# Kernel optimization log

Hardware: AMD Instinct MI355X
Metric: run time of the kernel (lower is better)

The kernel has to match this reference:

```python
import jax, jax.numpy as jnp
import numpy as np


def setup_inputs() -> dict:
    key = jax.random.key(0)
    k1, k2 = jax.random.split(key)
    B, IN, OUT = 4096, 4096, 4096
    x = jax.random.normal(k1, (B, IN), dtype=jnp.float32)
    W = jax.random.normal(k2, (OUT, IN), dtype=jnp.float32) * (1.0 / np.sqrt(IN))
    return {"x": x, "W": W, "k": 128}


def reference(x, W, k):
    # temp = (x[:, None, :] * W).sum(axis=1)  ==  x * W.sum(axis=0)  -> [B, in]
    # (the original materializes the O(B*out*in) intermediate; math is identical)
    temp = jax.lax.stop_gradient(x) * jnp.sum(W, axis=0)  # x_vals is detached in torch
    _, idx_top = jax.lax.top_k(jnp.abs(temp), k)          # [B, k] indices into `in` dim
    B = x.shape[0]
    z = jnp.ones_like(x).at[jnp.arange(B)[:, None], idx_top].set(0.0)
    out = jnp.matmul(x * z, W.T)                          # [B, out]
    return out
```

## Files before the change

### kernel.cpp

```cpp
#include <hip/hip_runtime.h>
#include <hip/hip_bf16.h>
#include <stdint.h>

#define B_DIM   4096
#define IN_DIM  4096
#define OUT_DIM 4096
#define K_SEL   128

typedef unsigned short u16;
typedef __bf16 bf16x8 __attribute__((ext_vector_type(8)));
typedef float  f32x4  __attribute__((ext_vector_type(4)));

static __device__ __forceinline__ u16 f2bf(float f) {
    uint32_t u = __builtin_bit_cast(uint32_t, f);
    uint32_t r = (u + 0x7fffu + ((u >> 16) & 1u)) >> 16;
    return (u16)r;
}

__global__ __launch_bounds__(256) void colsum_conv(const float* __restrict__ W,
                                                   double* __restrict__ part,
                                                   u16* __restrict__ Wb) {
    int cb = blockIdx.x & 15;
    int rb = blockIdx.x >> 4;
    int col = cb * 256 + threadIdx.x;
    int row0 = rb * 32;
    double s = 0.0;
    for (int r = 0; r < 32; ++r) {
        size_t idx = (size_t)(row0 + r) * IN_DIM + col;
        float v = W[idx];
        s += (double)v;
        Wb[idx] = f2bf(v);
    }
    part[(size_t)rb * IN_DIM + col] = s;
}

__global__ __launch_bounds__(256) void colsum_final(const double* __restrict__ part,
                                                    float* __restrict__ cs) {
    int col = blockIdx.x * 256 + threadIdx.x;
    double s = 0.0;
    for (int r = 0; r < 128; ++r) s += part[(size_t)r * IN_DIM + col];
    cs[col] = (float)s;
}

__global__ __launch_bounds__(256) void topk_mask(const float* __restrict__ x,
                                                 const float* __restrict__ cs,
                                                 u16* __restrict__ xz) {
    __shared__ uint32_t hist[256];
    __shared__ uint32_t suf[256];
    __shared__ uint32_t s_scan[256];
    __shared__ uint32_t s_prefix, s_krem;

    const int b = blockIdx.x, t = threadIdx.x;
    const float4* xrow = (const float4*)(x + (size_t)b * IN_DIM);
    const float4* csv  = (const float4*)cs;

    float    xr[16];
    uint32_t ul[16];
#pragma unroll
    for (int q = 0; q < 4; ++q) {
        float4 xv = xrow[t * 4 + q];
        float4 cv = csv[t * 4 + q];
        xr[q*4+0] = xv.x; xr[q*4+1] = xv.y; xr[q*4+2] = xv.z; xr[q*4+3] = xv.w;
        ul[q*4+0] = __builtin_bit_cast(uint32_t, xv.x * cv.x) & 0x7fffffffu;
        ul[q*4+1] = __builtin_bit_cast(uint32_t, xv.y * cv.y) & 0x7fffffffu;
        ul[q*4+2] = __builtin_bit_cast(uint32_t, xv.z * cv.z) & 0x7fffffffu;
        ul[q*4+3] = __builtin_bit_cast(uint32_t, xv.w * cv.w) & 0x7fffffffu;
    }
    if (t == 0) { s_prefix = 0u; s_krem = K_SEL; }
    __syncthreads();

#pragma unroll
    for (int p = 3; p >= 0; --p) {
        const int sh = p * 8;
        const uint32_t hi_mask = (p == 3) ? 0u : (0xFFFFFFFFu << (sh + 8));
        const uint32_t prefix = s_prefix;
        const uint32_t krem   = s_krem;
        hist[t] = 0u;
        __syncthreads();
#pragma unroll
        for (int j = 0; j < 16; ++j) {
            uint32_t u = ul[j];
            if ((u & hi_mask) == (prefix & hi_mask))
                atomicAdd(&hist[(u >> sh) & 255u], 1u);
        }
        __syncthreads();
        uint32_t mine = hist[t];
        suf[t] = mine;
        __syncthreads();
#pragma unroll
        for (int off = 1; off < 256; off <<= 1) {
            uint32_t other = (t + off < 256) ? suf[t + off] : 0u;
            __syncthreads();
            mine += other;
            suf[t] = mine;
            __syncthreads();
        }
        uint32_t mysuf   = suf[t];
        uint32_t nextsuf = (t < 255) ? suf[t + 1] : 0u;
        if (mysuf >= krem && (t == 255 || nextsuf < krem)) {
            s_prefix = prefix | ((uint32_t)t << sh);
            s_krem   = krem - nextsuf;
        }
        __syncthreads();
    }
    const uint32_t T       = s_prefix;
    const uint32_t need_eq = s_krem;

    int cnt = 0;
#pragma unroll
    for (int j = 0; j < 16; ++j) cnt += (ul[j] == T) ? 1 : 0;
    s_scan[t] = (uint32_t)cnt;
    __syncthreads();
    uint32_t inc = (uint32_t)cnt;
#pragma unroll
    for (int off = 1; off < 256; off <<= 1) {
        uint32_t other = (t >= off) ? s_scan[t - off] : 0u;
        __syncthreads();
        inc += other;
        s_scan[t] = inc;
        __syncthreads();
    }
    const int base = (int)(inc - (uint32_t)cnt);

    union { u16 us[16]; uint4 v[2]; } ob;
    int eqseen = 0;
#pragma unroll
    for (int j = 0; j < 16; ++j) {
        uint32_t u = ul[j];
        bool drop = (u > T);
        if (u == T) {
            if (base + eqseen < (int)need_eq) drop = true;
            ++eqseen;
        }
        ob.us[j] = drop ? (u16)0 : f2bf(xr[j]);
    }
    uint4* dst = (uint4*)(xz + (size_t)b * IN_DIM + t * 16);
    dst[0] = ob.v[0];
    dst[1] = ob.v[1];
}

#define NT 64

__global__ __launch_bounds__(512, 2) void gemm_8ph(const u16* __restrict__ A,
                                                   const u16* __restrict__ Bm,
                                                   float* __restrict__ C) {
    __shared__ u16 lds_[65536];

    const int bid = blockIdx.x;
    const int swz = (bid & 7) * 32 + (bid >> 3);
    const int m0 = (swz >> 4) * 256, n0 = (swz & 15) * 256;

    const int t = threadIdx.x;
    const int w = t >> 6, l = t & 63;
    const int lr = l & 15, lk = l >> 4;
    const int wm = w >> 2, wn = w & 3;

    const int cswz = ((t & 7) ^ ((t >> 3) & 7)) * 8;
    const int colA = (lk * 8) ^ ((lr & 7) * 8);

    f32x4 acc[8][4];
#pragma unroll
    for (int i = 0; i < 8; ++i)
#pragma unroll
        for (int j = 0; j < 4; ++j) acc[i][j] = f32x4{0.f, 0.f, 0.f, 0.f};

#define GLOAD(g, off_bytes)                                                     \
    __builtin_amdgcn_global_load_lds(                                           \
        (const __attribute__((address_space(1))) void*)(g),                     \
        (__attribute__((address_space(3))) void*)(((char*)lds_) + (off_bytes)), \
        16, 0, 0)

    auto stA = [&](int kb, int s, int kt) {
        GLOAD(A + (size_t)(m0 + s * 64 + (t >> 3)) * IN_DIM + kt + cswz,
              kb * 65536 + s * 8192 + t * 16);
    };
    auto stB = [&](int kb, int s, int kt) {
        GLOAD(Bm + (size_t)(n0 + s * 64 + (t >> 3)) * IN_DIM + kt + cswz,
              kb * 65536 + 32768 + s * 8192 + t * 16);
    };

    stA(0, 0, 0); stA(0, 1, 0); stA(0, 2, 0); stA(0, 3, 0);
    stB(0, 0, 0); stB(0, 1, 0); stB(0, 2, 0); stB(0, 3, 0);
    stA(1, 0, 64); stA(1, 2, 64);
    asm volatile("s_waitcnt vmcnt(2)" ::: "memory");
    __builtin_amdgcn_s_barrier();
    asm volatile("" ::: "memory");

    for (int k = 0; k < NT; ++k) {
        const int buf = k & 1, bufn = buf ^ 1;
        const int kt1 = (k + 1) * 64;
        const int ktc = (k + 2 < NT ? k + 2 : NT - 1) * 64;
        const int Ab = buf * 32768 + (wm * 2) * 4096;
        const int Bb = buf * 32768 + 16384 + wn * 4096;
#pragma unroll
        for (int p = 0; p < 4; ++p) {
            const int q = p >> 1, ks = p & 1;
            const int col = colA ^ (ks * 32);
            bf16x8 a[4], b[4];
            const int ra = Ab + q * 4096 + lr * 64 + col;
#pragma unroll
            for (int mi = 0; mi < 4; ++mi)
                a[mi] = *(const bf16x8*)&lds_[ra + mi * 1024];
            const int rb = Bb + lr * 64 + col;
#pragma unroll
            for (int ni = 0; ni < 4; ++ni)
                b[ni] = *(const bf16x8*)&lds_[rb + ni * 1024];

            if (p == 0) {
                if (k < NT - 1) { stB(bufn, 0, kt1); stB(bufn, 1, kt1);
                                  stA(bufn, 1, kt1); stA(bufn, 3, kt1); }
            } else if (p == 1) {
                if (k < NT - 1) { stB(bufn, 2, kt1); stB(bufn, 3, kt1); }
            } else if (p == 2) {
                stA(buf, 0, ktc); stA(buf, 2, ktc);
            }
            asm volatile("" ::: "memory");
            __builtin_amdgcn_s_barrier();
            asm volatile("s_waitcnt lgkmcnt(0)" ::: "memory");
            __builtin_amdgcn_sched_barrier(0);
            __builtin_amdgcn_s_setprio(1);
#pragma unroll
            for (int mi = 0; mi < 4; ++mi)
#pragma unroll
                for (int ni = 0; ni < 4; ++ni)
                    acc[q * 4 + mi][ni] = __builtin_amdgcn_mfma_f32_16x16x32_bf16(
                        a[mi], b[ni], acc[q * 4 + mi][ni], 0, 0, 0);
            __builtin_amdgcn_s_setprio(0);
            __builtin_amdgcn_sched_barrier(0);
            if (p == 3) asm volatile("s_waitcnt vmcnt(2)" ::: "memory");
            asm volatile("" ::: "memory");
            __builtin_amdgcn_s_barrier();
            asm volatile("" ::: "memory");
        }
    }
#undef GLOAD

#pragma unroll
    for (int gmi = 0; gmi < 8; ++gmi)
#pragma unroll
        for (int ni = 0; ni < 4; ++ni)
#pragma unroll
            for (int r = 0; r < 4; ++r) {
                int row = m0 + wm * 128 + (gmi >> 2) * 64 + (gmi & 3) * 16 + lk * 4 + r;
                int col = n0 + wn * 64 + ni * 16 + lr;
                C[(size_t)row * OUT_DIM + col] = acc[gmi][ni][r];
            }
}

extern "C" void kernel_launch(void* const* d_in, const int* in_sizes, int n_in,
                              void* d_out, int out_size, void* d_ws, size_t ws_size,
                              hipStream_t stream) {
    const float* x = (const float*)d_in[0];
    const float* W = (const float*)d_in[1];
    float* out = (float*)d_out;

    char* ws = (char*)d_ws;
    u16*    Wb   = (u16*)ws;
    u16*    xz   = (u16*)(ws + (size_t)32 * 1024 * 1024);
    float*  cs   = (float*)(ws + (size_t)64 * 1024 * 1024);
    double* part = (double*)d_out;

    colsum_conv<<<2048, 256, 0, stream>>>(W, part, Wb);
    colsum_final<<<16, 256, 0, stream>>>(part, cs);
    topk_mask<<<4096, 256, 0, stream>>>(x, cs, xz);
    gemm_8ph<<<256, 512, 0, stream>>>(xz, Wb, out);
}
```

Before: 195.2 us.

## Restructure GEMM main loop into quadrant phases with register reuse of A/B fragments

Rewrites the bf16 GEMM inner loop so each K-tile runs four quadrant phases (A-top×B-left, A-top×B-right, A-bottom×B-left, A-bottom×B-right). Loaded A and B fragments are reused across phases, which cuts LDS reads per tile. The LDS layout and global-to-LDS load order change so the next tiles are prefetched per quadrant, interleaved with the MFMA blocks and tracked by new vmcnt/lgkmcnt waits. The aim is fewer LDS reads and better overlap of loads with MFMAs. The cost is more fragile synchronisation and higher register pressure from holding A and both B halves at once.

After: 189.3 us. -3.0%, faster.

```diff
diff --git a/kernel.cpp b/kernel.cpp
--- a/kernel.cpp
+++ b/kernel.cpp
@@ -156,7 +156,7 @@
     const int wm = w >> 2, wn = w & 3;
 
     const int cswz = ((t & 7) ^ ((t >> 3) & 7)) * 8;
-    const int colA = (lk * 8) ^ ((lr & 7) * 8);
+    const int c0   = (lk ^ (lr & 7)) * 8;
 
     f32x4 acc[8][4];
 #pragma unroll
@@ -169,71 +169,131 @@
         (const __attribute__((address_space(1))) void*)(g),                     \
         (__attribute__((address_space(3))) void*)(((char*)lds_) + (off_bytes)), \
         16, 0, 0)
-
-    auto stA = [&](int kb, int s, int kt) {
-        GLOAD(A + (size_t)(m0 + s * 64 + (t >> 3)) * IN_DIM + kt + cswz,
-              kb * 65536 + s * 8192 + t * 16);
+#define MFMA_(d, va, vb) d = __builtin_amdgcn_mfma_f32_16x16x32_bf16(va, vb, d, 0, 0, 0)
+
+    auto stA = [&](int b, int qm, int kt) {
+#pragma unroll
+        for (int g = 0; g < 2; ++g)
+            GLOAD(A + (size_t)(m0 + g * 128 + qm * 64 + (t >> 3)) * IN_DIM + kt + cswz,
+                  b * 65536 + qm * 16384 + g * 8192 + t * 16);
     };
-    auto stB = [&](int kb, int s, int kt) {
-        GLOAD(Bm + (size_t)(n0 + s * 64 + (t >> 3)) * IN_DIM + kt + cswz,
-              kb * 65536 + 32768 + s * 8192 + t * 16);
+    auto stB = [&](int b, int qn, int kt) {
+#pragma unroll
+        for (int g = 0; g < 2; ++g)
+            GLOAD(Bm + (size_t)(n0 + (g * 2 + (t >> 8)) * 64 + qn * 32 + ((t >> 3) & 31)) * IN_DIM + kt + cswz,
+                  b * 65536 + 32768 + qn * 16384 + g * 8192 + t * 16);
     };
 
-    stA(0, 0, 0); stA(0, 1, 0); stA(0, 2, 0); stA(0, 3, 0);
-    stB(0, 0, 0); stB(0, 1, 0); stB(0, 2, 0); stB(0, 3, 0);
-    stA(1, 0, 64); stA(1, 2, 64);
-    asm volatile("s_waitcnt vmcnt(2)" ::: "memory");
+    stA(0, 0, 0); stB(0, 0, 0); stA(0, 1, 0); stB(0, 1, 0);
+    stA(1, 0, 64); stB(1, 0, 64); stA(1, 1, 64);
+    asm volatile("s_waitcnt vmcnt(6)" ::: "memory");
     __builtin_amdgcn_s_barrier();
     asm volatile("" ::: "memory");
 
     for (int k = 0; k < NT; ++k) {
         const int buf = k & 1, bufn = buf ^ 1;
-        const int kt1 = (k + 1) * 64;
-        const int ktc = (k + 2 < NT ? k + 2 : NT - 1) * 64;
-        const int Ab = buf * 32768 + (wm * 2) * 4096;
-        const int Bb = buf * 32768 + 16384 + wn * 4096;
-#pragma unroll
-        for (int p = 0; p < 4; ++p) {
-            const int q = p >> 1, ks = p & 1;
-            const int col = colA ^ (ks * 32);
-            bf16x8 a[4], b[4];
-            const int ra = Ab + q * 4096 + lr * 64 + col;
-#pragma unroll
-            for (int mi = 0; mi < 4; ++mi)
-                a[mi] = *(const bf16x8*)&lds_[ra + mi * 1024];
-            const int rb = Bb + lr * 64 + col;
-#pragma unroll
-            for (int ni = 0; ni < 4; ++ni)
-                b[ni] = *(const bf16x8*)&lds_[rb + ni * 1024];
-
-            if (p == 0) {
-                if (k < NT - 1) { stB(bufn, 0, kt1); stB(bufn, 1, kt1);
-                                  stA(bufn, 1, kt1); stA(bufn, 3, kt1); }
-            } else if (p == 1) {
-                if (k < NT - 1) { stB(bufn, 2, kt1); stB(bufn, 3, kt1); }
-            } else if (p == 2) {
-                stA(buf, 0, ktc); stA(buf, 2, ktc);
-            }
-            asm volatile("" ::: "memory");
-            __builtin_amdgcn_s_barrier();
-            asm volatile("s_waitcnt lgkmcnt(0)" ::: "memory");
-            __builtin_amdgcn_sched_barrier(0);
-            __builtin_amdgcn_s_setprio(1);
-#pragma unroll
-            for (int mi = 0; mi < 4; ++mi)
-#pragma unroll
-                for (int ni = 0; ni < 4; ++ni)
-                    acc[q * 4 + mi][ni] = __builtin_amdgcn_mfma_f32_16x16x32_bf16(
-                        a[mi], b[ni], acc[q * 4 + mi][ni], 0, 0, 0);
-            __builtin_amdgcn_s_setprio(0);
-            __builtin_amdgcn_sched_barrier(0);
-            if (p == 3) asm volatile("s_waitcnt vmcnt(2)" ::: "memory");
-            asm volatile("" ::: "memory");
-            __builtin_amdgcn_s_barrier();
-            asm volatile("" ::: "memory");
-        }
+        const int kt1 = (k + 1 < NT ? k + 1 : NT - 1) * 64;
+        const int kt2 = (k + 2 < NT ? k + 2 : NT - 1) * 64;
+        const int aB = buf * 32768 + (wm * 64 + lr) * 64;
+        const int bB = buf * 32768 + 16384 + (wn * 32 + lr) * 64;
+
+        bf16x8 a[4][2], b0[2][2], b1[2][2];
+
+#pragma unroll
+        for (int mi = 0; mi < 4; ++mi) {
+            a[mi][0] = *(const bf16x8*)&lds_[aB + mi * 1024 + c0];
+            a[mi][1] = *(const bf16x8*)&lds_[aB + mi * 1024 + (c0 ^ 32)];
+        }
+#pragma unroll
+        for (int ni = 0; ni < 2; ++ni) {
+            b0[ni][0] = *(const bf16x8*)&lds_[bB + ni * 1024 + c0];
+            b0[ni][1] = *(const bf16x8*)&lds_[bB + ni * 1024 + (c0 ^ 32)];
+        }
+        stB(bufn, 1, kt1);
+        asm volatile("s_waitcnt lgkmcnt(8)" ::: "memory");
+        __builtin_amdgcn_s_barrier();
+        asm volatile("s_waitcnt lgkmcnt(0)" ::: "memory");
+        __builtin_amdgcn_sched_barrier(0);
+        __builtin_amdgcn_s_setprio(1);
+#pragma unroll
+        for (int mi = 0; mi < 4; ++mi)
+#pragma unroll
+            for (int ni = 0; ni < 2; ++ni) {
+                MFMA_(acc[mi][ni], a[mi][0], b0[ni][0]);
+                MFMA_(acc[mi][ni], a[mi][1], b0[ni][1]);
+            }
+        __builtin_amdgcn_s_setprio(0);
+        __builtin_amdgcn_sched_barrier(0);
+        asm volatile("" ::: "memory");
+        __builtin_amdgcn_s_barrier();
+        asm volatile("" ::: "memory");
+
+#pragma unroll
+        for (int ni = 0; ni < 2; ++ni) {
+            b1[ni][0] = *(const bf16x8*)&lds_[bB + 8192 + ni * 1024 + c0];
+            b1[ni][1] = *(const bf16x8*)&lds_[bB + 8192 + ni * 1024 + (c0 ^ 32)];
+        }
+        stA(buf, 0, kt2);
+        asm volatile("" ::: "memory");
+        __builtin_amdgcn_s_barrier();
+        asm volatile("s_waitcnt lgkmcnt(0)" ::: "memory");
+        __builtin_amdgcn_sched_barrier(0);
+        __builtin_amdgcn_s_setprio(1);
+#pragma unroll
+        for (int mi = 0; mi < 4; ++mi)
+#pragma unroll
+            for (int ni = 0; ni < 2; ++ni) {
+                MFMA_(acc[mi][2 + ni], a[mi][0], b1[ni][0]);
+                MFMA_(acc[mi][2 + ni], a[mi][1], b1[ni][1]);
+            }
+        __builtin_amdgcn_s_setprio(0);
+        __builtin_amdgcn_sched_barrier(0);
+        asm volatile("" ::: "memory");
+        __builtin_amdgcn_s_barrier();
+        asm volatile("" ::: "memory");
+
+#pragma unroll
+        for (int mi = 0; mi < 4; ++mi) {
+            a[mi][0] = *(const bf16x8*)&lds_[aB + 8192 + mi * 1024 + c0];
+            a[mi][1] = *(const bf16x8*)&lds_[aB + 8192 + mi * 1024 + (c0 ^ 32)];
+        }
+        stB(buf, 0, kt2);
+        asm volatile("" ::: "memory");
+        __builtin_amdgcn_s_barrier();
+        asm volatile("s_waitcnt lgkmcnt(0)" ::: "memory");
+        __builtin_amdgcn_sched_barrier(0);
+        __builtin_amdgcn_s_setprio(1);
+#pragma unroll
+        for (int mi = 0; mi < 4; ++mi)
+#pragma unroll
+            for (int ni = 0; ni < 2; ++ni) {
+                MFMA_(acc[4 + mi][ni], a[mi][0], b0[ni][0]);
+                MFMA_(acc[4 + mi][ni], a[mi][1], b0[ni][1]);
+            }
+        __builtin_amdgcn_s_setprio(0);
+        __builtin_amdgcn_sched_barrier(0);
+        asm volatile("" ::: "memory");
+        __builtin_amdgcn_s_barrier();
+        asm volatile("" ::: "memory");
+
+        stA(buf, 1, kt2);
+        asm volatile("" ::: "memory");
+        __builtin_amdgcn_s_setprio(1);
+#pragma unroll
+        for (int mi = 0; mi < 4; ++mi)
+#pragma unroll
+            for (int ni = 0; ni < 2; ++ni) {
+                MFMA_(acc[4 + mi][2 + ni], a[mi][0], b1[ni][0]);
+                MFMA_(acc[4 + mi][2 + ni], a[mi][1], b1[ni][1]);
+            }
+        __builtin_amdgcn_s_setprio(0);
+        __builtin_amdgcn_sched_barrier(0);
+        asm volatile("s_waitcnt vmcnt(6)" ::: "memory");
+        __builtin_amdgcn_s_barrier();
+        asm volatile("" ::: "memory");
     }
 #undef GLOAD
+#undef MFMA_
 
 #pragma unroll
     for (int gmi = 0; gmi < 8; ++gmi)
```

## Software-pipeline GEMM LDS reads with MFMA and vectorize column-sum kernel

Applied to the files above, without the earlier changes.

The GEMM main loop is restructured so LDS fragment reads for the next sub-step are issued while the MFMA block of the current sub-step runs. It uses ping-pong register fragments, a new LDS layout for the A/B halves, and fewer barriers per k-tile. The column-sum/convert kernel now loads float4 and stores ushort4/double4, with 8 rows per block and 512 partial rows. This trades higher register pressure and a longer final reduction loop for better overlap and vectorized memory access.

After: 204.3 us. 4.7% more time.

```diff
diff --git a/kernel.cpp b/kernel.cpp
--- a/kernel.cpp
+++ b/kernel.cpp
@@ -20,25 +20,27 @@
 __global__ __launch_bounds__(256) void colsum_conv(const float* __restrict__ W,
                                                    double* __restrict__ part,
                                                    u16* __restrict__ Wb) {
-    int cb = blockIdx.x & 15;
-    int rb = blockIdx.x >> 4;
-    int col = cb * 256 + threadIdx.x;
-    int row0 = rb * 32;
-    double s = 0.0;
-    for (int r = 0; r < 32; ++r) {
-        size_t idx = (size_t)(row0 + r) * IN_DIM + col;
-        float v = W[idx];
-        s += (double)v;
-        Wb[idx] = f2bf(v);
-    }
-    part[(size_t)rb * IN_DIM + col] = s;
+    int cb = blockIdx.x & 3;
+    int rb = blockIdx.x >> 2;
+    int c4 = cb * 256 + threadIdx.x;
+    int row0 = rb * 8;
+    double s0 = 0.0, s1 = 0.0, s2 = 0.0, s3 = 0.0;
+    for (int r = 0; r < 8; ++r) {
+        const float4 v = ((const float4*)(W + (size_t)(row0 + r) * IN_DIM))[c4];
+        s0 += (double)v.x; s1 += (double)v.y; s2 += (double)v.z; s3 += (double)v.w;
+        ushort4 o;
+        o.x = f2bf(v.x); o.y = f2bf(v.y); o.z = f2bf(v.z); o.w = f2bf(v.w);
+        ((ushort4*)(Wb + (size_t)(row0 + r) * IN_DIM))[c4] = o;
+    }
+    double4 d; d.x = s0; d.y = s1; d.z = s2; d.w = s3;
+    ((double4*)(part + (size_t)rb * IN_DIM))[c4] = d;
 }
 
 __global__ __launch_bounds__(256) void colsum_final(const double* __restrict__ part,
                                                     float* __restrict__ cs) {
     int col = blockIdx.x * 256 + threadIdx.x;
     double s = 0.0;
-    for (int r = 0; r < 128; ++r) s += part[(size_t)r * IN_DIM + col];
+    for (int r = 0; r < 512; ++r) s += part[(size_t)r * IN_DIM + col];
     cs[col] = (float)s;
 }
 
@@ -141,9 +143,9 @@
 
 #define NT 64
 
-__global__ __launch_bounds__(512, 2) void gemm_8ph(const u16* __restrict__ A,
-                                                   const u16* __restrict__ Bm,
-                                                   float* __restrict__ C) {
+__global__ __launch_bounds__(512, 2) void gemm_pl(const u16* __restrict__ A,
+                                                  const u16* __restrict__ Bm,
+                                                  float* __restrict__ C) {
     __shared__ u16 lds_[65536];
 
     const int bid = blockIdx.x;
@@ -151,12 +153,14 @@
     const int m0 = (swz >> 4) * 256, n0 = (swz & 15) * 256;
 
     const int t = threadIdx.x;
-    const int w = t >> 6, l = t & 63;
+    const int l = t & 63;
     const int lr = l & 15, lk = l >> 4;
+    const int w = t >> 6;
     const int wm = w >> 2, wn = w & 3;
 
     const int cswz = ((t & 7) ^ ((t >> 3) & 7)) * 8;
-    const int colA = (lk * 8) ^ ((lr & 7) * 8);
+    const int c0   = (lk ^ (lr & 7)) * 8;
+    const int c1   = c0 ^ 32;
 
     f32x4 acc[8][4];
 #pragma unroll
@@ -170,68 +174,89 @@
         (__attribute__((address_space(3))) void*)(((char*)lds_) + (off_bytes)), \
         16, 0, 0)
 
-    auto stA = [&](int kb, int s, int kt) {
-        GLOAD(A + (size_t)(m0 + s * 64 + (t >> 3)) * IN_DIM + kt + cswz,
-              kb * 65536 + s * 8192 + t * 16);
-    };
-    auto stB = [&](int kb, int s, int kt) {
-        GLOAD(Bm + (size_t)(n0 + s * 64 + (t >> 3)) * IN_DIM + kt + cswz,
-              kb * 65536 + 32768 + s * 8192 + t * 16);
-    };
-
-    stA(0, 0, 0); stA(0, 1, 0); stA(0, 2, 0); stA(0, 3, 0);
-    stB(0, 0, 0); stB(0, 1, 0); stB(0, 2, 0); stB(0, 3, 0);
-    stA(1, 0, 64); stA(1, 2, 64);
-    asm volatile("s_waitcnt vmcnt(2)" ::: "memory");
+    auto stA = [&](int kb, int qm, int kt) {
+#pragma unroll
+        for (int g = 0; g < 2; ++g)
+            GLOAD(A + (size_t)(m0 + g * 128 + qm * 64 + (t >> 3)) * IN_DIM + kt + cswz,
+                  kb * 65536 + qm * 16384 + g * 8192 + t * 16);
+    };
+    auto stB = [&](int kb, int qn, int kt) {
+#pragma unroll
+        for (int g = 0; g < 2; ++g)
+            GLOAD(Bm + (size_t)(n0 + (g * 2 + (t >> 8)) * 64 + qn * 32 + ((t >> 3) & 31)) * IN_DIM + kt + cswz,
+                  kb * 65536 + 32768 + qn * 16384 + g * 8192 + t * 16);
+    };
+
+    auto rdA = [&](bf16x8 (&dst)[4], int bufo, int qm, int c) {
+#pragma unroll
+        for (int mi = 0; mi < 4; ++mi)
+            dst[mi] = *(const bf16x8*)&lds_[bufo + qm * 8192 + wm * 4096 + lr * 64 + mi * 1024 + c];
+    };
+    auto rdB = [&](bf16x8 (&dst)[4], int bufo, int c) {
+#pragma unroll
+        for (int ni = 0; ni < 4; ++ni)
+            dst[ni] = *(const bf16x8*)&lds_[bufo + 16384 + (ni >> 1) * 8192 + wn * 2048 + lr * 64 + (ni & 1) * 1024 + c];
+    };
+    auto mm = [&](int base, bf16x8 (&Aa)[4], bf16x8 (&Bb)[4]) {
+#pragma unroll
+        for (int mi = 0; mi < 4; ++mi)
+#pragma unroll
+            for (int ni = 0; ni < 4; ++ni)
+                acc[base + mi][ni] = __builtin_amdgcn_mfma_f32_16x16x32_bf16(
+                    Aa[mi], Bb[ni], acc[base + mi][ni], 0, 0, 0);
+    };
+
+    bf16x8 aX[4], aY[4], bX[4], bY[4];
+
+    stA(0, 0, 0); stA(0, 1, 0); stB(0, 0, 0); stB(0, 1, 0);
+    asm volatile("s_waitcnt vmcnt(0)" ::: "memory");
     __builtin_amdgcn_s_barrier();
     asm volatile("" ::: "memory");
+    rdA(aX, 0, 0, c0);
+    rdB(bX, 0, c0);
 
     for (int k = 0; k < NT; ++k) {
-        const int buf = k & 1, bufn = buf ^ 1;
-        const int kt1 = (k + 1) * 64;
-        const int ktc = (k + 2 < NT ? k + 2 : NT - 1) * 64;
-        const int Ab = buf * 32768 + (wm * 2) * 4096;
-        const int Bb = buf * 32768 + 16384 + wn * 4096;
-#pragma unroll
-        for (int p = 0; p < 4; ++p) {
-            const int q = p >> 1, ks = p & 1;
-            const int col = colA ^ (ks * 32);
-            bf16x8 a[4], b[4];
-            const int ra = Ab + q * 4096 + lr * 64 + col;
-#pragma unroll
-            for (int mi = 0; mi < 4; ++mi)
-                a[mi] = *(const bf16x8*)&lds_[ra + mi * 1024];
-            const int rb = Bb + lr * 64 + col;
-#pragma unroll
-            for (int ni = 0; ni < 4; ++ni)
-                b[ni] = *(const bf16x8*)&lds_[rb + ni * 1024];
-
-            if (p == 0) {
-                if (k < NT - 1) { stB(bufn, 0, kt1); stB(bufn, 1, kt1);
-                                  stA(bufn, 1, kt1); stA(bufn, 3, kt1); }
-            } else if (p == 1) {
-                if (k < NT - 1) { stB(bufn, 2, kt1); stB(bufn, 3, kt1); }
-            } else if (p == 2) {
-                stA(buf, 0, ktc); stA(buf, 2, ktc);
-            }
-            asm volatile("" ::: "memory");
-            __builtin_amdgcn_s_barrier();
-            asm volatile("s_waitcnt lgkmcnt(0)" ::: "memory");
-            __builtin_amdgcn_sched_barrier(0);
-            __builtin_amdgcn_s_setprio(1);
-#pragma unroll
-            for (int mi = 0; mi < 4; ++mi)
-#pragma unroll
-                for (int ni = 0; ni < 4; ++ni)
-                    acc[q * 4 + mi][ni] = __builtin_amdgcn_mfma_f32_16x16x32_bf16(
-                        a[mi], b[ni], acc[q * 4 + mi][ni], 0, 0, 0);
-            __builtin_amdgcn_s_setprio(0);
-            __builtin_amdgcn_sched_barrier(0);
-            if (p == 3) asm volatile("s_waitcnt vmcnt(2)" ::: "memory");
-            asm volatile("" ::: "memory");
-            __builtin_amdgcn_s_barrier();
-            asm volatile("" ::: "memory");
-        }
+        const int bufo = (k & 1) * 32768, bufno = bufo ^ 32768;
+        const int kbn  = (k & 1) ^ 1;
+        const int kt1  = (k + 1) * 64;
+
+        rdA(aY, bufo, 1, c0);
+        if (k < NT - 1) {
+            stA(kbn, 0, kt1); stA(kbn, 1, kt1);
+            stB(kbn, 0, kt1); stB(kbn, 1, kt1);
+        }
+        __builtin_amdgcn_s_setprio(1);
+        mm(0, aX, bX);
+        __builtin_amdgcn_s_setprio(0);
+        __builtin_amdgcn_sched_barrier(0);
+
+        rdA(aX, bufo, 0, c1);
+        rdB(bY, bufo, c1);
+        __builtin_amdgcn_s_setprio(1);
+        mm(4, aY, bX);
+        __builtin_amdgcn_s_setprio(0);
+        __builtin_amdgcn_sched_barrier(0);
+
+        rdA(aY, bufo, 1, c1);
+        __builtin_amdgcn_s_setprio(1);
+        mm(0, aX, bY);
+        __builtin_amdgcn_s_setprio(0);
+        __builtin_amdgcn_sched_barrier(0);
+        asm volatile("s_waitcnt vmcnt(0)" ::: "memory");
+        __builtin_amdgcn_s_barrier();
+        asm volatile("" ::: "memory");
+
+        if (k < NT - 1) {
+            rdA(aX, bufno, 0, c0);
+            rdB(bX, bufno, c0);
+        }
+        __builtin_amdgcn_s_setprio(1);
+        mm(4, aY, bY);
+        __builtin_amdgcn_s_setprio(0);
+        __builtin_amdgcn_sched_barrier(0);
+        asm volatile("" ::: "memory");
+        __builtin_amdgcn_s_barrier();
+        asm volatile("" ::: "memory");
     }
 #undef GLOAD
 
@@ -263,5 +288,5 @@
     colsum_conv<<<2048, 256, 0, stream>>>(W, part, Wb);
     colsum_final<<<16, 256, 0, stream>>>(part, cs);
     topk_mask<<<4096, 256, 0, stream>>>(x, cs, xz);
-    gemm_8ph<<<256, 512, 0, stream>>>(xz, Wb, out);
-}
+    gemm_pl<<<256, 512, 0, stream>>>(xz, Wb, out);
+}
```
